# Kernel tuning notes

Hardware: AMD Instinct MI355X
Metric: run time of the kernel (lower is better)

Reference implementation:

```python
import jax, jax.numpy as jnp
import numpy as np

B, N, DIM_X, DIM_E = 16, 2048, 512, 64


def setup_inputs() -> dict:
    key = jax.random.key(0)
    kx, ke, k0, k1, k2, k3 = jax.random.split(key, 6)
    s = lambda fan_in: 1.0 / np.sqrt(fan_in)
    return {
        "x": jax.random.normal(kx, (B, N, DIM_X), dtype=jnp.float32),
        "e": jax.random.normal(ke, (N, DIM_E), dtype=jnp.float32),
        # nn.Linear weights: shape [out_features, in_features], U(-1/sqrt(in), 1/sqrt(in))
        "W0": jax.random.uniform(k0, (DIM_X, DIM_X), jnp.float32, -s(DIM_X), s(DIM_X)),  # W_Q_W_KT
        "W1": jax.random.uniform(k1, (DIM_E, DIM_X), jnp.float32, -s(DIM_X), s(DIM_X)),  # Wx_Q_We_KT
        "W2": jax.random.uniform(k2, (DIM_X, DIM_E), jnp.float32, -s(DIM_E), s(DIM_E)),  # We_Q_Wx_KT
        "W3": jax.random.uniform(k3, (DIM_E, DIM_E), jnp.float32, -s(DIM_E), s(DIM_E)),  # We_Q_We_KT
    }


def reference(x, e, W0, W1, W2, W3):
    # causal_temporal_map='lower_triangle': weight <- relu(triu(weight, 1))
    W0m = jax.nn.relu(jnp.triu(W0, 1))
    # attn0 = (x @ W0m.T) @ x^T over time axis t   -> [b, n, m]
    attn0 = jnp.einsum("bnt,bmt->bnm", x @ W0m.T, x)
    # e is shared across batch (repeat); keep it 2D and broadcast
    attn1 = jnp.einsum("bne,me->bnm", x @ W1.T, e)        # Wx_Q_We_KT(x) . e
    attn2 = jnp.einsum("nt,bmt->bnm", e @ W2.T, x)        # We_Q_Wx_KT(e) . x
    attn3 = jnp.einsum("ne,me->nm", e @ W3.T, e)          # We_Q_We_KT(e) . e, batch-shared
    attn = attn0 + attn1 + attn2 + attn3[None]            # dropout p=0.0 -> identity
    # v = x.clone(); out = attn @ v
    out = jnp.einsum("bnm,bmt->bnt", attn, x)
    return out
```

## Files before the change

### kernel.cpp

```cpp
#include <hip/hip_runtime.h>
#include <hip/hip_bf16.h>


typedef __attribute__((ext_vector_type(8))) short s16x8;
typedef __attribute__((ext_vector_type(4))) short s16x4;
typedef __attribute__((ext_vector_type(4))) float f32x4;

__device__ __forceinline__ unsigned short f2bf(float f) {
  union { float f; unsigned u; } v; v.f = f;
  unsigned r = v.u + 0x7fff + ((v.u >> 16) & 1);
  return (unsigned short)(r >> 16);
}

template<int TM, int TN, int GX, int GY, int OUT_F32, int KSW>
__global__ __launch_bounds__(256) void gemm_nt(
    const unsigned short* __restrict__ A, long sAb, int lda,
    const unsigned short* __restrict__ A2, int lda2,
    const unsigned short* __restrict__ B, long sBb, int ldb,
    void* __restrict__ Cptr, long sCb, int ldc,
    int K)
{
  constexpr int TK = 64;
  constexpr int WM = TM / 2, WN = TN / 2;
  constexpr int AM = WM / 16, AN = WN / 16;
  constexpr int ACH = TM / 8;
  constexpr int BCH = TN / 8;
  constexpr int NBLK = GX * GY;

  __shared__ unsigned short As[2][TM * TK];
  __shared__ unsigned short Bs[2][TN * TK];

  const int bid  = blockIdx.x;
  const int xcd  = bid & 7;
  const int slot = bid >> 3;
  const int bz   = xcd + 8 * (slot / NBLK);
  const int tix  = slot % NBLK;
  const int m0   = (tix % GX) * TM;
  const int n0   = (tix / GX) * TN;

  const unsigned short* Ab = A + (long)bz * sAb;
  const unsigned short* Bb = B + (long)bz * sBb;

  const int tid  = threadIdx.x;
  const int lane = tid & 63;
  const int wave = tid >> 6;
  const int wm = (wave >> 1) * WM;
  const int wn = (wave & 1) * WN;
  const int fr = lane & 15;
  const int fg = lane >> 4;
  const int fx = fr & 7;

  const int srow = lane >> 3;
  const int scol = (((lane & 7) ^ (lane >> 3)) & 7) * 8;

  f32x4 acc[AM][AN];
#pragma unroll
  for (int i = 0; i < AM; i++)
#pragma unroll
    for (int j = 0; j < AN; j++) acc[i][j] = (f32x4)(0.f);

  auto stage = [&](int buf, int t) {
    const int k0 = t * TK;
    const unsigned short* asrc;
    int asl;
    if (KSW >= 0 && t >= KSW) { asrc = A2 + (k0 - KSW * TK); asl = lda2; }
    else                      { asrc = Ab + k0;              asl = lda;  }
#pragma unroll
    for (int i = 0; i < ACH / 4; i++) {
      const int c = wave * (ACH / 4) + i;
      __builtin_amdgcn_global_load_lds(
          (const __attribute__((address_space(1))) unsigned*)
              (asrc + (long)(m0 + c * 8 + srow) * asl + scol),
          (__attribute__((address_space(3))) unsigned*)(&As[buf][c * 512]),
          16, 0, 0);
    }
#pragma unroll
    for (int i = 0; i < BCH / 4; i++) {
      const int c = wave * (BCH / 4) + i;
      __builtin_amdgcn_global_load_lds(
          (const __attribute__((address_space(1))) unsigned*)
              (Bb + (long)(n0 + c * 8 + srow) * ldb + k0 + scol),
          (__attribute__((address_space(3))) unsigned*)(&Bs[buf][c * 512]),
          16, 0, 0);
    }
  };

  const int NT = K / TK;
  stage(0, 0);
  __syncthreads();

  for (int t = 0; t < NT; ++t) {
    const int cur = t & 1;
    if (t + 1 < NT) stage(cur ^ 1, t + 1);

    const unsigned short* Ac = &As[cur][0];
    const unsigned short* Bc = &Bs[cur][0];
#pragma unroll
    for (int ks = 0; ks < 2; ks++) {
      s16x8 av[AM], bv[AN];
#pragma unroll
      for (int mt = 0; mt < AM; mt++)
        av[mt] = *(const s16x8*)
            &Ac[(wm + mt * 16 + fr) * TK + (((ks * 4 + fg) ^ fx) * 8)];
#pragma unroll
      for (int nt = 0; nt < AN; nt++)
        bv[nt] = *(const s16x8*)
            &Bc[(wn + nt * 16 + fr) * TK + (((ks * 4 + fg) ^ fx) * 8)];
#pragma unroll
      for (int mt = 0; mt < AM; mt++)
#pragma unroll
        for (int nt = 0; nt < AN; nt++)
          acc[mt][nt] = __builtin_amdgcn_mfma_f32_16x16x32_bf16(
              av[mt], bv[nt], acc[mt][nt], 0, 0, 0);
    }
    __syncthreads();
  }

  if (OUT_F32) {
    float* C = (float*)Cptr + (long)bz * sCb;
#pragma unroll
    for (int mt = 0; mt < AM; mt++) {
      const int row = m0 + wm + mt * 16 + fg * 4;
#pragma unroll
      for (int nt = 0; nt < AN; nt++) {
        const int col = n0 + wn + nt * 16 + fr;
#pragma unroll
        for (int j = 0; j < 4; j++)
          C[(long)(row + j) * ldc + col] = acc[mt][nt][j];
      }
    }
  } else {
    unsigned short* C = (unsigned short*)Cptr + (long)bz * sCb;
#pragma unroll
    for (int mt = 0; mt < AM; mt++) {
      const int row = m0 + wm + mt * 16 + fg * 4;
#pragma unroll
      for (int nt = 0; nt < AN; nt++) {
        const int col = n0 + wn + nt * 16 + fr;
#pragma unroll
        for (int j = 0; j < 4; j++)
          C[(long)(row + j) * ldc + col] = f2bf(acc[mt][nt][j]);
      }
    }
  }
}

__global__ __launch_bounds__(256) void convert_fused(
    const float* __restrict__ x, const float* __restrict__ e,
    const float* __restrict__ W0, const float* __restrict__ W1,
    const float* __restrict__ W2, const float* __restrict__ W3,
    unsigned short* __restrict__ XeT, unsigned short* __restrict__ Xb,
    unsigned short* __restrict__ eb, unsigned short* __restrict__ Wb)
{
  constexpr int KP = 66;
  __shared__ unsigned short t[64 * KP];

  if (blockIdx.z >= 16) {
    const int tidx = (blockIdx.z - 16) * 288 + blockIdx.y * 32 + blockIdx.x;
    if (tidx >= 324) return;
    float* tw = (float*)t;
    const int m0 = (tidx / 18) * 32;
    const int k0 = (tidx % 18) * 32;
    const int r  = threadIdx.x >> 3;
    const int c4 = (threadIdx.x & 7) * 4;

    const int k = k0 + r;
    float4 v;
    if (m0 < 512) {
      if (k0 < 512) v = *(const float4*)&W0[k * 512 + m0 + c4];
      else          v = *(const float4*)&W1[(k - 512) * 512 + m0 + c4];
    } else {
      if (k0 < 512) v = *(const float4*)&W2[k * 64 + (m0 - 512) + c4];
      else          v = *(const float4*)&W3[(k - 512) * 64 + (m0 - 512) + c4];
    }
    tw[r * 33 + c4 + 0] = v.x; tw[r * 33 + c4 + 1] = v.y;
    tw[r * 33 + c4 + 2] = v.z; tw[r * 33 + c4 + 3] = v.w;
    __syncthreads();

    const int m = m0 + r;
    const bool tri = (m0 < 512) && (k0 < 512);
    s16x4 o;
#pragma unroll
    for (int j = 0; j < 4; ++j) {
      const int kk = k0 + c4 + j;
      float val = tw[(c4 + j) * 33 + r];
      if (tri) val = (m > kk) ? fmaxf(val, 0.f) : 0.f;
      o[j] = f2bf(val);
    }
    *(s16x4*)&Wb[m * 576 + k0 + c4] = o;
    return;
  }

  const int b  = blockIdx.z;
  const int k0 = blockIdx.x * 64;
  const int f0 = blockIdx.y * 64;
  const bool isE = (f0 >= 512);
  const int l  = threadIdx.x & 63;
  const int w  = threadIdx.x >> 6;
  const int fi = (l & 15) * 4;

#pragma unroll
  for (int it = 0; it < 4; ++it) {
    const int row = w * 16 + it * 4 + (l >> 4);
    const int k = k0 + row;
    float4 v = isE ? *(const float4*)&e[(long)k * 64 + fi]
                   : *(const float4*)&x[((long)b * 2048 + k) * 512 + f0 + fi];
    s16x4 o; o[0] = f2bf(v.x); o[1] = f2bf(v.y); o[2] = f2bf(v.z); o[3] = f2bf(v.w);
    if (isE) { if (b == 0) *(s16x4*)&eb[(long)k * 64 + fi] = o; }
    else     *(s16x4*)&Xb[((long)b * 2048 + k) * 512 + f0 + fi] = o;
    t[(fi + 0) * KP + row] = o[0];
    t[(fi + 1) * KP + row] = o[1];
    t[(fi + 2) * KP + row] = o[2];
    t[(fi + 3) * KP + row] = o[3];
  }
  __syncthreads();

  const int fr = threadIdx.x >> 2;
  const int kq = (threadIdx.x & 3) * 8;
  const s16x8 o0 = *(const s16x8*)&t[fr * KP + kq];
  const s16x8 o1 = *(const s16x8*)&t[fr * KP + kq + 32];
  const long obase = ((long)b * 576 + f0 + fr) * 2048 + k0;
  *(s16x8*)&XeT[obase + kq]      = o0;
  *(s16x8*)&XeT[obase + kq + 32] = o1;
}

extern "C" void kernel_launch(void* const* d_in, const int* in_sizes, int n_in,
                              void* d_out, int out_size, void* d_ws, size_t ws_size,
                              hipStream_t stream) {
  const float* x  = (const float*)d_in[0];
  const float* e  = (const float*)d_in[1];
  const float* W0 = (const float*)d_in[2];
  const float* W1 = (const float*)d_in[3];
  const float* W2 = (const float*)d_in[4];
  const float* W3 = (const float*)d_in[5];
  float* out = (float*)d_out;

  const size_t SZ_XeT = (size_t)16 * 576 * 2048 * 2;
  const size_t SZ_CT  = (size_t)16 * 512 * 576 * 2;
  const size_t SZ_DT  = SZ_CT;
  const size_t SZ_WB  = (size_t)576 * 576 * 2;
  const size_t SZ_XB  = (size_t)16 * 2048 * 512 * 2;
  const size_t SZ_EB  = (size_t)2048 * 64 * 2;

  char* p = (char*)d_ws;
  unsigned short* XeT = (unsigned short*)p;  p += SZ_XeT;
  unsigned short* CT  = (unsigned short*)p;  p += SZ_CT;
  unsigned short* DT  = (unsigned short*)p;  p += SZ_DT;
  unsigned short* Wb  = (unsigned short*)p;  p += SZ_WB;
  unsigned short* Xb  = (unsigned short*)p;  p += SZ_XB;
  unsigned short* eb  = (unsigned short*)p;  p += SZ_EB;
  const size_t base = SZ_XeT + SZ_CT + SZ_DT + SZ_WB + SZ_XB + SZ_EB;
  if (ws_size < base) return;

  convert_fused<<<dim3(32, 9, 18), 256, 0, stream>>>(
      x, e, W0, W1, W2, W3, XeT, Xb, eb, Wb);

  gemm_nt<64, 96, 8, 6, 0, -1><<<768, 256, 0, stream>>>(
      XeT, (long)576 * 2048, 2048, nullptr, 0,
      XeT, (long)576 * 2048, 2048,
      CT,  (long)512 * 576, 576, 2048);

  gemm_nt<64, 96, 8, 6, 0, -1><<<768, 256, 0, stream>>>(
      CT, (long)512 * 576, 576, nullptr, 0,
      Wb, 0L, 576,
      DT, (long)512 * 576, 576, 576);

  gemm_nt<128, 128, 16, 4, 1, 8><<<1024, 256, 0, stream>>>(
      Xb, (long)2048 * 512, 512, eb, 64,
      DT, (long)512 * 576, 576,
      out, (long)2048 * 512, 512, 576);
}
```

Baseline: 89.03 us.

## Split-K the first GEMM into two halves and sum partials in the second GEMM's A load

```diff
diff --git a/kernel.cpp b/kernel.cpp
--- a/kernel.cpp
+++ b/kernel.cpp
@@ -12,20 +12,20 @@
   return (unsigned short)(r >> 16);
 }
 
-template<int TM, int TN, int GX, int GY, int OUT_F32, int KSW>
+template<int TM, int TN, int GX, int GY, int OUT_F32, int KSW, int SPK, int SUM2>
 __global__ __launch_bounds__(256) void gemm_nt(
     const unsigned short* __restrict__ A, long sAb, int lda,
     const unsigned short* __restrict__ A2, int lda2,
     const unsigned short* __restrict__ B, long sBb, int ldb,
     void* __restrict__ Cptr, long sCb, int ldc,
-    int K)
+    int K, long sSP)
 {
   constexpr int TK = 64;
   constexpr int WM = TM / 2, WN = TN / 2;
   constexpr int AM = WM / 16, AN = WN / 16;
   constexpr int ACH = TM / 8;
   constexpr int BCH = TN / 8;
-  constexpr int NBLK = GX * GY;
+  constexpr int NBLK = GX * GY * (SPK ? 2 : 1);
 
   __shared__ unsigned short As[2][TM * TK];
   __shared__ unsigned short Bs[2][TN * TK];
@@ -35,11 +35,15 @@
   const int slot = bid >> 3;
   const int bz   = xcd + 8 * (slot / NBLK);
   const int tix  = slot % NBLK;
-  const int m0   = (tix % GX) * TM;
-  const int n0   = (tix / GX) * TN;
-
-  const unsigned short* Ab = A + (long)bz * sAb;
-  const unsigned short* Bb = B + (long)bz * sBb;
+  int sp = 0, tix0 = tix;
+  if (SPK) { sp = tix / (GX * GY); tix0 = tix % (GX * GY); }
+  const int m0 = (tix0 % GX) * TM;
+  const int n0 = (tix0 / GX) * TN;
+  const int kbase = sp * K;
+
+  const unsigned short* Ab  = A + (long)bz * sAb;
+  const unsigned short* Bb  = B + (long)bz * sBb;
+  const unsigned short* A2b = SUM2 ? (A2 + (long)bz * sAb) : A2;
 
   const int tid  = threadIdx.x;
   const int lane = tid & 63;
@@ -60,26 +64,44 @@
     for (int j = 0; j < AN; j++) acc[i][j] = (f32x4)(0.f);
 
   auto stage = [&](int buf, int t) {
-    const int k0 = t * TK;
-    const unsigned short* asrc;
-    int asl;
-    if (KSW >= 0 && t >= KSW) { asrc = A2 + (k0 - KSW * TK); asl = lda2; }
-    else                      { asrc = Ab + k0;              asl = lda;  }
-#pragma unroll
-    for (int i = 0; i < ACH / 4; i++) {
-      const int c = wave * (ACH / 4) + i;
-      __builtin_amdgcn_global_load_lds(
-          (const __attribute__((address_space(1))) unsigned*)
-              (asrc + (long)(m0 + c * 8 + srow) * asl + scol),
-          (__attribute__((address_space(3))) unsigned*)(&As[buf][c * 512]),
-          16, 0, 0);
+    const int k0 = kbase + t * TK;
+    if (SUM2) {
+#pragma unroll
+      for (int i = 0; i < ACH / 4; i++) {
+        const int c = wave * (ACH / 4) + i;
+        const long off = (long)(m0 + c * 8 + srow) * lda + k0 + scol;
+        const s16x8 va = *(const s16x8*)&Ab[off];
+        const s16x8 vb = *(const s16x8*)&A2b[off];
+        s16x8 o;
+#pragma unroll
+        for (int j = 0; j < 8; ++j) {
+          const float fa = __uint_as_float(((unsigned)(unsigned short)va[j]) << 16);
+          const float fb = __uint_as_float(((unsigned)(unsigned short)vb[j]) << 16);
+          o[j] = f2bf(fa + fb);
+        }
+        *(s16x8*)&As[buf][c * 512 + lane * 8] = o;
+      }
+    } else {
+      const unsigned short* asrc;
+      int asl;
+      if (KSW >= 0 && t >= KSW) { asrc = A2 + (k0 - KSW * TK); asl = lda2; }
+      else                      { asrc = Ab + k0;              asl = lda;  }
+#pragma unroll
+      for (int i = 0; i < ACH / 4; i++) {
+        const int c = wave * (ACH / 4) + i;
+        __builtin_amdgcn_global_load_lds(
+            (const __attribute__((address_space(1))) unsigned*)
+                (asrc + (long)(m0 + c * 8 + srow) * asl + scol),
+            (__attribute__((address_space(3))) unsigned*)(&As[buf][c * 512]),
+            16, 0, 0);
+      }
     }
 #pragma unroll
     for (int i = 0; i < BCH / 4; i++) {
       const int c = wave * (BCH / 4) + i;
       __builtin_amdgcn_global_load_lds(
           (const __attribute__((address_space(1))) unsigned*)
-              (Bb + (long)(n0 + c * 8 + srow) * ldb + k0 + scol),
+              (Bb + (long)(n0 + c * 8 + srow) * ldb + kbase + t * TK + scol),
           (__attribute__((address_space(3))) unsigned*)(&Bs[buf][c * 512]),
           16, 0, 0);
     }
@@ -117,7 +139,7 @@
   }
 
   if (OUT_F32) {
-    float* C = (float*)Cptr + (long)bz * sCb;
+    float* C = (float*)Cptr + (long)bz * sCb + (long)sp * sSP;
 #pragma unroll
     for (int mt = 0; mt < AM; mt++) {
       const int row = m0 + wm + mt * 16 + fg * 4;
@@ -130,7 +152,7 @@
       }
     }
   } else {
-    unsigned short* C = (unsigned short*)Cptr + (long)bz * sCb;
+    unsigned short* C = (unsigned short*)Cptr + (long)bz * sCb + (long)sp * sSP;
 #pragma unroll
     for (int mt = 0; mt < AM; mt++) {
       const int row = m0 + wm + mt * 16 + fg * 4;
@@ -244,29 +266,30 @@
 
   char* p = (char*)d_ws;
   unsigned short* XeT = (unsigned short*)p;  p += SZ_XeT;
-  unsigned short* CT  = (unsigned short*)p;  p += SZ_CT;
+  unsigned short* CTa = (unsigned short*)p;  p += SZ_CT;
+  unsigned short* CTb = (unsigned short*)p;  p += SZ_CT;
   unsigned short* DT  = (unsigned short*)p;  p += SZ_DT;
   unsigned short* Wb  = (unsigned short*)p;  p += SZ_WB;
   unsigned short* Xb  = (unsigned short*)p;  p += SZ_XB;
   unsigned short* eb  = (unsigned short*)p;  p += SZ_EB;
-  const size_t base = SZ_XeT + SZ_CT + SZ_DT + SZ_WB + SZ_XB + SZ_EB;
+  const size_t base = SZ_XeT + 2 * SZ_CT + SZ_DT + SZ_WB + SZ_XB + SZ_EB;
   if (ws_size < base) return;
 
   convert_fused<<<dim3(32, 9, 18), 256, 0, stream>>>(
       x, e, W0, W1, W2, W3, XeT, Xb, eb, Wb);
 
-  gemm_nt<64, 96, 8, 6, 0, -1><<<768, 256, 0, stream>>>(
+  gemm_nt<128, 96, 4, 6, 0, -1, 1, 0><<<768, 256, 0, stream>>>(
       XeT, (long)576 * 2048, 2048, nullptr, 0,
       XeT, (long)576 * 2048, 2048,
-      CT,  (long)512 * 576, 576, 2048);
-
-  gemm_nt<64, 96, 8, 6, 0, -1><<<768, 256, 0, stream>>>(
-      CT, (long)512 * 576, 576, nullptr, 0,
+      CTa, (long)512 * 576, 576, 1024, (long)16 * 512 * 576);
+
+  gemm_nt<64, 96, 8, 6, 0, -1, 0, 1><<<768, 256, 0, stream>>>(
+      CTa, (long)512 * 576, 576, CTb, 0,
       Wb, 0L, 576,
-      DT, (long)512 * 576, 576, 576);
-
-  gemm_nt<128, 128, 16, 4, 1, 8><<<1024, 256, 0, stream>>>(
+      DT, (long)512 * 576, 576, 576, 0);
+
+  gemm_nt<128, 128, 16, 4, 1, 8, 0, 0><<<1024, 256, 0, stream>>>(
       Xb, (long)2048 * 512, 512, eb, 64,
       DT, (long)512 * 576, 576,
-      out, (long)2048 * 512, 512, 576);
-}
+      out, (long)2048 * 512, 512, 576, 0);
+}
```

After: 95.64 us. 7.4% more time.
